# Performance work log

Measured on AMD Instinct MI355X. Metric: run time of the kernel, lower is better.

Reference implementation:

```python
import jax, jax.numpy as jnp
import numpy as np

S = 14
STEP = 1.0 / S
LAMBDA_COORD = 7.0
LAMBDA_NOOBJ = 0.2
LAMBDA_CLS = 1.5
EPS = 1e-06


def _abs_coords(boxes):
    # boxes: [N, S, S, 2, 5] -> [N, S, S, 2, 4] (x1,y1,x2,y2)
    ys, xs = jnp.meshgrid(jnp.arange(S, dtype=boxes.dtype), jnp.arange(S, dtype=boxes.dtype), indexing='ij')
    xg = xs[None, :, :, None]
    yg = ys[None, :, :, None]
    cx = (boxes[..., 0] + xg) * STEP
    cy = (boxes[..., 1] + yg) * STEP
    w = boxes[..., 2]
    h = boxes[..., 3]
    return jnp.stack([cx - w / 2, cy - h / 2, cx + w / 2, cy + h / 2], axis=-1)


def _iou(b1, b2):
    x1 = jnp.maximum(b1[..., 0], b2[..., 0])
    y1 = jnp.maximum(b1[..., 1], b2[..., 1])
    x2 = jnp.minimum(b1[..., 2], b2[..., 2])
    y2 = jnp.minimum(b1[..., 3], b2[..., 3])
    inter = jnp.clip(x2 - x1, 0) * jnp.clip(y2 - y1, 0)
    a1 = (b1[..., 2] - b1[..., 0]) * (b1[..., 3] - b1[..., 1])
    a2 = (b2[..., 2] - b2[..., 0]) * (b2[..., 3] - b2[..., 1])
    return inter / (a1 + a2 - inter + EPS)


def _ciou_loss(b1, b2):
    iou = _iou(b1, b2)
    cx1 = (b1[..., 0] + b1[..., 2]) / 2
    cy1 = (b1[..., 1] + b1[..., 3]) / 2
    cx2 = (b2[..., 0] + b2[..., 2]) / 2
    cy2 = (b2[..., 1] + b2[..., 3]) / 2
    center_dist = (cx1 - cx2) ** 2 + (cy1 - cy2) ** 2
    xc1 = jnp.minimum(b1[..., 0], b2[..., 0])
    yc1 = jnp.minimum(b1[..., 1], b2[..., 1])
    xc2 = jnp.maximum(b1[..., 2], b2[..., 2])
    yc2 = jnp.maximum(b1[..., 3], b2[..., 3])
    outer_diag = (xc2 - xc1) ** 2 + (yc2 - yc1) ** 2 + EPS
    w1 = jnp.clip(b1[..., 2] - b1[..., 0], EPS)
    h1 = jnp.clip(b1[..., 3] - b1[..., 1], EPS)
    w2 = jnp.clip(b2[..., 2] - b2[..., 0], EPS)
    h2 = jnp.clip(b2[..., 3] - b2[..., 1], EPS)
    v = (4.0 / jnp.pi ** 2) * (jnp.arctan(w2 / h2) - jnp.arctan(w1 / h1)) ** 2
    alpha = v / (1 - iou + v + EPS)
    ciou = iou - center_dist / outer_diag - alpha * v
    scale = jnp.clip(2 - w2 * h2, 1.0)
    return (1 - ciou) * scale


def setup_inputs() -> dict:
    key = jax.random.key(0)
    k1, k2 = jax.random.split(key)
    N = 4096
    pred = jax.random.uniform(k1, (N, S, S, 30), dtype=jnp.float32)
    target = jax.random.uniform(k2, (N, S, S, 30), dtype=jnp.float32)
    return {"pred": pred, "target": target}


def reference(pred, target):
    N = pred.shape[0]
    tb = target[..., :10].reshape(N, S, S, 2, 5)
    pb = pred[..., :10].reshape(N, S, S, 2, 5)
    tcls = target[..., 10:]
    pcls = pred[..., 10:]

    obj = tb[..., 4] > 0                      # [N,S,S,2]
    pabs = _abs_coords(pb)                    # [N,S,S,2,4]
    tabs = _abs_coords(tb)

    # responsible-box assignment: IoU of both pred boxes vs target box 0
    ious = _iou(pabs, tabs[..., 0:1, :])      # [N,S,S,2]
    max_i = jnp.argmax(ious, axis=-1)         # first-max tie-break, same as torch
    resp = max_i[..., None] == jnp.arange(2)  # [N,S,S,2] bool
    obj = obj & resp
    noobj = ~obj

    pconf = pb[..., 4]
    tconf = tb[..., 4]
    se = (pconf - tconf) ** 2
    noobj_loss = jnp.sum(se * noobj)
    obj_loss = jnp.sum(se * obj)

    bbox_loss = jnp.sum(_ciou_loss(pabs, tabs) * obj)

    sig = jnp.any(obj, axis=-1)               # [N,S,S]
    # torch F.binary_cross_entropy clamps log terms at -100
    logp = jnp.clip(jnp.log(pcls), -100.0)
    log1mp = jnp.clip(jnp.log1p(-pcls), -100.0)
    bce = -(tcls * logp + (1 - tcls) * log1mp)
    class_loss = jnp.sum(bce * sig[..., None]) * LAMBDA_CLS

    loss = obj_loss + LAMBDA_NOOBJ * noobj_loss + LAMBDA_COORD * bbox_loss + class_loss
    return loss / N
```

## Files before the change

### kernel.cpp

```cpp
#include <hip/hip_runtime.h>
#include <math.h>

namespace {
constexpr int SG = 14;
constexpr int NIMG = 4096;
constexpr int NCELLS = NIMG * SG * SG;
constexpr int CPB = 256;
constexpr int PAD = 31;
constexpr float STEPF = 1.0f / 14.0f;
constexpr float EPSF = 1e-6f;
constexpr float L_COORD = 7.0f;
constexpr float L_NOOBJ = 0.2f;
constexpr float L_CLS = 1.5f;
constexpr float INV_N = 1.0f / 4096.0f;
constexpr float FOUR_OVER_PI2 = 4.0f / (float)(M_PI * M_PI);
}

struct Box { float x1, y1, x2, y2; };

__device__ __forceinline__ float iou_fn(const Box& a, const Box& b) {
  float ix1 = fmaxf(a.x1, b.x1);
  float iy1 = fmaxf(a.y1, b.y1);
  float ix2 = fminf(a.x2, b.x2);
  float iy2 = fminf(a.y2, b.y2);
  float inter = fmaxf(ix2 - ix1, 0.0f) * fmaxf(iy2 - iy1, 0.0f);
  float a1 = (a.x2 - a.x1) * (a.y2 - a.y1);
  float a2 = (b.x2 - b.x1) * (b.y2 - b.y1);
  return inter / (a1 + a2 - inter + EPSF);
}

__global__ __launch_bounds__(256) void yolo_loss_kernel(
    const float* __restrict__ pred, const float* __restrict__ tgt,
    float* __restrict__ out) {
  __shared__ float lp[CPB * PAD];
  __shared__ float lt[CPB * PAD];

  const int tid = threadIdx.x;

  {
    const float2* P2 = reinterpret_cast<const float2*>(pred) + (size_t)blockIdx.x * (CPB * 30 / 2);
    const float2* T2 = reinterpret_cast<const float2*>(tgt)  + (size_t)blockIdx.x * (CPB * 30 / 2);
#pragma unroll
    for (int j = 0; j < 15; ++j) {
      const int idx = j * 256 + tid;
      const int f = idx * 2;
      const int c = f / 30;
      const int e = f - 30 * c;
      const float2 v = P2[idx];
      lp[c * PAD + e] = v.x; lp[c * PAD + e + 1] = v.y;
      const float2 u = T2[idx];
      lt[c * PAD + e] = u.x; lt[c * PAD + e + 1] = u.y;
    }
  }
  __syncthreads();

  float p[30], t[30];
#pragma unroll
  for (int k = 0; k < 30; ++k) { p[k] = lp[tid * PAD + k]; t[k] = lt[tid * PAD + k]; }

  const int cell = blockIdx.x * CPB + tid;
  const int rem = cell % (SG * SG);
  const float gx = (float)(rem % SG);
  const float gy = (float)(rem / SG);

  Box pa0, pa1, ta0, ta1;
  {
    float cx = (p[0] + gx) * STEPF, cy = (p[1] + gy) * STEPF, w = p[2], h = p[3];
    pa0 = {cx - 0.5f * w, cy - 0.5f * h, cx + 0.5f * w, cy + 0.5f * h};
    cx = (p[5] + gx) * STEPF; cy = (p[6] + gy) * STEPF; w = p[7]; h = p[8];
    pa1 = {cx - 0.5f * w, cy - 0.5f * h, cx + 0.5f * w, cy + 0.5f * h};
    cx = (t[0] + gx) * STEPF; cy = (t[1] + gy) * STEPF; w = t[2]; h = t[3];
    ta0 = {cx - 0.5f * w, cy - 0.5f * h, cx + 0.5f * w, cy + 0.5f * h};
    cx = (t[5] + gx) * STEPF; cy = (t[6] + gy) * STEPF; w = t[7]; h = t[8];
    ta1 = {cx - 0.5f * w, cy - 0.5f * h, cx + 0.5f * w, cy + 0.5f * h};
  }

  const float iou0 = iou_fn(pa0, ta0);
  const float iou1 = iou_fn(pa1, ta0);
  const bool m1 = iou1 > iou0;
  const bool obj0 = (t[4] > 0.0f) && !m1;
  const bool obj1 = (t[9] > 0.0f) && m1;
  const bool sig = obj0 || obj1;

  const float d0 = p[4] - t[4], d1 = p[9] - t[9];
  const float se0 = d0 * d0, se1 = d1 * d1;
  const float obj_loss   = (obj0 ? se0 : 0.0f) + (obj1 ? se1 : 0.0f);
  const float noobj_loss = (obj0 ? 0.0f : se0) + (obj1 ? 0.0f : se1);

  Box b1, b2;
  b1.x1 = m1 ? pa1.x1 : pa0.x1; b1.y1 = m1 ? pa1.y1 : pa0.y1;
  b1.x2 = m1 ? pa1.x2 : pa0.x2; b1.y2 = m1 ? pa1.y2 : pa0.y2;
  b2.x1 = m1 ? ta1.x1 : ta0.x1; b2.y1 = m1 ? ta1.y1 : ta0.y1;
  b2.x2 = m1 ? ta1.x2 : ta0.x2; b2.y2 = m1 ? ta1.y2 : ta0.y2;

  float bbox;
  {
    const float iou = iou_fn(b1, b2);
    const float cx1 = 0.5f * (b1.x1 + b1.x2), cy1 = 0.5f * (b1.y1 + b1.y2);
    const float cx2 = 0.5f * (b2.x1 + b2.x2), cy2 = 0.5f * (b2.y1 + b2.y2);
    const float cd = (cx1 - cx2) * (cx1 - cx2) + (cy1 - cy2) * (cy1 - cy2);
    const float ox1 = fminf(b1.x1, b2.x1), oy1 = fminf(b1.y1, b2.y1);
    const float ox2 = fmaxf(b1.x2, b2.x2), oy2 = fmaxf(b1.y2, b2.y2);
    const float od = (ox2 - ox1) * (ox2 - ox1) + (oy2 - oy1) * (oy2 - oy1) + EPSF;
    const float w1 = fmaxf(b1.x2 - b1.x1, EPSF), h1 = fmaxf(b1.y2 - b1.y1, EPSF);
    const float w2 = fmaxf(b2.x2 - b2.x1, EPSF), h2 = fmaxf(b2.y2 - b2.y1, EPSF);
    const float dat = atanf(w2 / h2) - atanf(w1 / h1);
    const float v = FOUR_OVER_PI2 * dat * dat;
    const float alpha = v / (1.0f - iou + v + EPSF);
    const float ciou = iou - cd / od - alpha * v;
    const float scale = fmaxf(2.0f - w2 * h2, 1.0f);
    bbox = sig ? (1.0f - ciou) * scale : 0.0f;
  }

  float cls = 0.0f;
#pragma unroll
  for (int k = 10; k < 30; ++k) {
    const float pc = p[k], tc = t[k];
    const float lp_  = fmaxf(logf(pc), -100.0f);
    const float l1mp = fmaxf(log1pf(-pc), -100.0f);
    cls += -(tc * lp_ + (1.0f - tc) * l1mp);
  }

  float acc = obj_loss + L_NOOBJ * noobj_loss + L_COORD * bbox
            + (sig ? L_CLS * cls : 0.0f);

#pragma unroll
  for (int off = 32; off > 0; off >>= 1) acc += __shfl_down(acc, off);

  __shared__ float sdata[4];
  const int lane = tid & 63;
  const int wid  = tid >> 6;
  if (lane == 0) sdata[wid] = acc;
  __syncthreads();
  if (tid == 0) {
    const float s = sdata[0] + sdata[1] + sdata[2] + sdata[3];
    atomicAdd(out, s * INV_N);
  }
}

extern "C" void kernel_launch(void* const* d_in, const int* in_sizes, int n_in,
                              void* d_out, int out_size, void* d_ws, size_t ws_size,
                              hipStream_t stream) {
  const float* pred = (const float*)d_in[0];
  const float* tgt  = (const float*)d_in[1];
  float* out = (float*)d_out;

  hipMemsetAsync(out, 0, sizeof(float), stream);

  const int blocks = NCELLS / CPB;
  yolo_loss_kernel<<<blocks, CPB, 0, stream>>>(pred, tgt, out);
}
```

Before: 217.6 us.

## Share one LDS buffer for pred and target, use fast math intrinsics

```diff
diff --git a/kernel.cpp b/kernel.cpp
--- a/kernel.cpp
+++ b/kernel.cpp
@@ -26,37 +26,51 @@
   float inter = fmaxf(ix2 - ix1, 0.0f) * fmaxf(iy2 - iy1, 0.0f);
   float a1 = (a.x2 - a.x1) * (a.y2 - a.y1);
   float a2 = (b.x2 - b.x1) * (b.y2 - b.y1);
-  return inter / (a1 + a2 - inter + EPSF);
+  return __fdividef(inter, a1 + a2 - inter + EPSF);
 }
 
 __global__ __launch_bounds__(256) void yolo_loss_kernel(
     const float* __restrict__ pred, const float* __restrict__ tgt,
     float* __restrict__ out) {
-  __shared__ float lp[CPB * PAD];
-  __shared__ float lt[CPB * PAD];
+  __shared__ float buf[CPB * PAD];
+  __shared__ float sdata[4];
 
   const int tid = threadIdx.x;
 
   {
-    const float2* P2 = reinterpret_cast<const float2*>(pred) + (size_t)blockIdx.x * (CPB * 30 / 2);
-    const float2* T2 = reinterpret_cast<const float2*>(tgt)  + (size_t)blockIdx.x * (CPB * 30 / 2);
+    const float2* P2 = reinterpret_cast<const float2*>(pred) + (size_t)blockIdx.x * (CPB * 15);
 #pragma unroll
     for (int j = 0; j < 15; ++j) {
       const int idx = j * 256 + tid;
-      const int f = idx * 2;
-      const int c = f / 30;
-      const int e = f - 30 * c;
+      const int c = idx / 15;
+      const int addr = 2 * idx + c;
       const float2 v = P2[idx];
-      lp[c * PAD + e] = v.x; lp[c * PAD + e + 1] = v.y;
-      const float2 u = T2[idx];
-      lt[c * PAD + e] = u.x; lt[c * PAD + e + 1] = u.y;
+      buf[addr] = v.x; buf[addr + 1] = v.y;
     }
   }
   __syncthreads();
 
-  float p[30], t[30];
+  float p[30];
 #pragma unroll
-  for (int k = 0; k < 30; ++k) { p[k] = lp[tid * PAD + k]; t[k] = lt[tid * PAD + k]; }
+  for (int k = 0; k < 30; ++k) p[k] = buf[tid * PAD + k];
+  __syncthreads();
+
+  {
+    const float2* T2 = reinterpret_cast<const float2*>(tgt) + (size_t)blockIdx.x * (CPB * 15);
+#pragma unroll
+    for (int j = 0; j < 15; ++j) {
+      const int idx = j * 256 + tid;
+      const int c = idx / 15;
+      const int addr = 2 * idx + c;
+      const float2 u = T2[idx];
+      buf[addr] = u.x; buf[addr + 1] = u.y;
+    }
+  }
+  __syncthreads();
+
+  float tb[10];
+#pragma unroll
+  for (int k = 0; k < 10; ++k) tb[k] = buf[tid * PAD + k];
 
   const int cell = blockIdx.x * CPB + tid;
   const int rem = cell % (SG * SG);
@@ -69,20 +83,20 @@
     pa0 = {cx - 0.5f * w, cy - 0.5f * h, cx + 0.5f * w, cy + 0.5f * h};
     cx = (p[5] + gx) * STEPF; cy = (p[6] + gy) * STEPF; w = p[7]; h = p[8];
     pa1 = {cx - 0.5f * w, cy - 0.5f * h, cx + 0.5f * w, cy + 0.5f * h};
-    cx = (t[0] + gx) * STEPF; cy = (t[1] + gy) * STEPF; w = t[2]; h = t[3];
+    cx = (tb[0] + gx) * STEPF; cy = (tb[1] + gy) * STEPF; w = tb[2]; h = tb[3];
     ta0 = {cx - 0.5f * w, cy - 0.5f * h, cx + 0.5f * w, cy + 0.5f * h};
-    cx = (t[5] + gx) * STEPF; cy = (t[6] + gy) * STEPF; w = t[7]; h = t[8];
+    cx = (tb[5] + gx) * STEPF; cy = (tb[6] + gy) * STEPF; w = tb[7]; h = tb[8];
     ta1 = {cx - 0.5f * w, cy - 0.5f * h, cx + 0.5f * w, cy + 0.5f * h};
   }
 
   const float iou0 = iou_fn(pa0, ta0);
   const float iou1 = iou_fn(pa1, ta0);
   const bool m1 = iou1 > iou0;
-  const bool obj0 = (t[4] > 0.0f) && !m1;
-  const bool obj1 = (t[9] > 0.0f) && m1;
+  const bool obj0 = (tb[4] > 0.0f) && !m1;
+  const bool obj1 = (tb[9] > 0.0f) && m1;
   const bool sig = obj0 || obj1;
 
-  const float d0 = p[4] - t[4], d1 = p[9] - t[9];
+  const float d0 = p[4] - tb[4], d1 = p[9] - tb[9];
   const float se0 = d0 * d0, se1 = d1 * d1;
   const float obj_loss   = (obj0 ? se0 : 0.0f) + (obj1 ? se1 : 0.0f);
   const float noobj_loss = (obj0 ? 0.0f : se0) + (obj1 ? 0.0f : se1);
@@ -104,21 +118,22 @@
     const float od = (ox2 - ox1) * (ox2 - ox1) + (oy2 - oy1) * (oy2 - oy1) + EPSF;
     const float w1 = fmaxf(b1.x2 - b1.x1, EPSF), h1 = fmaxf(b1.y2 - b1.y1, EPSF);
     const float w2 = fmaxf(b2.x2 - b2.x1, EPSF), h2 = fmaxf(b2.y2 - b2.y1, EPSF);
-    const float dat = atanf(w2 / h2) - atanf(w1 / h1);
+    const float dat = atanf(__fdividef(w2, h2)) - atanf(__fdividef(w1, h1));
     const float v = FOUR_OVER_PI2 * dat * dat;
-    const float alpha = v / (1.0f - iou + v + EPSF);
-    const float ciou = iou - cd / od - alpha * v;
+    const float alpha = __fdividef(v, 1.0f - iou + v + EPSF);
+    const float ciou = iou - __fdividef(cd, od) - alpha * v;
     const float scale = fmaxf(2.0f - w2 * h2, 1.0f);
     bbox = sig ? (1.0f - ciou) * scale : 0.0f;
   }
 
   float cls = 0.0f;
 #pragma unroll
-  for (int k = 10; k < 30; ++k) {
-    const float pc = p[k], tc = t[k];
-    const float lp_  = fmaxf(logf(pc), -100.0f);
-    const float l1mp = fmaxf(log1pf(-pc), -100.0f);
-    cls += -(tc * lp_ + (1.0f - tc) * l1mp);
+  for (int k = 0; k < 20; ++k) {
+    const float pc = p[10 + k];
+    const float tc = buf[tid * PAD + 10 + k];
+    const float lg   = fmaxf(__logf(pc), -100.0f);
+    const float l1mp = fmaxf(__logf(1.0f - pc), -100.0f);
+    cls += -(tc * lg + (1.0f - tc) * l1mp);
   }
 
   float acc = obj_loss + L_NOOBJ * noobj_loss + L_COORD * bbox
@@ -127,7 +142,6 @@
 #pragma unroll
   for (int off = 32; off > 0; off >>= 1) acc += __shfl_down(acc, off);
 
-  __shared__ float sdata[4];
   const int lane = tid & 63;
   const int wid  = tid >> 6;
   if (lane == 0) sdata[wid] = acc;
```

New measurement: 207.6 us. 4.6% less time.
